# Optimization experiments

Hardware: AMD Instinct MI355X
Metric: run time of the kernel (lower is better)

## Reference

```python
import jax, jax.numpy as jnp
import numpy as np

B, H, W, C = 8, 28, 28, 1024
NH = 16
HD = C // NH          # head dim 64
HID = 4 * C           # mlp hidden 4096
BC = C // 2           # bottleneck channels 512
SCALE = HD ** -0.5


def setup_inputs() -> dict:
    key = jax.random.key(0)
    ks = iter(jax.random.split(key, 32))
    def rn(shape, s=0.02):
        return jax.random.normal(next(ks), shape, jnp.float32) * s
    return dict(
        x=jax.random.normal(next(ks), (B, H, W, C), jnp.float32),
        norm1_w=jnp.ones((C,), jnp.float32), norm1_b=jnp.zeros((C,), jnp.float32),
        qkv_w=rn((C, 3 * C)), qkv_b=jnp.zeros((3 * C,), jnp.float32),
        proj_w=rn((C, C)), proj_b=jnp.zeros((C,), jnp.float32),
        rel_h=rn((2 * H - 1, HD)), rel_w=rn((2 * W - 1, HD)),
        norm2_w=jnp.ones((C,), jnp.float32), norm2_b=jnp.zeros((C,), jnp.float32),
        fc1_w=rn((C, HID)), fc1_b=jnp.zeros((HID,), jnp.float32),
        fc2_w=rn((HID, C)), fc2_b=jnp.zeros((C,), jnp.float32),
        conv1_w=rn((1, 1, C, BC)), ln1_w=jnp.ones((BC,), jnp.float32), ln1_b=jnp.zeros((BC,), jnp.float32),
        conv2_w=rn((3, 3, BC, BC)), ln2_w=jnp.ones((BC,), jnp.float32), ln2_b=jnp.zeros((BC,), jnp.float32),
        conv3_w=rn((1, 1, BC, C)), ln3_w=rn((C,)), ln3_b=rn((C,)),
    )


def _ln(x, w, b, eps):
    # layernorm over last axis (channels in NHWC)
    m = jnp.mean(x, -1, keepdims=True)
    v = jnp.mean((x - m) ** 2, -1, keepdims=True)
    return (x - m) * jax.lax.rsqrt(v + eps) * w + b


def _conv(x, w, pad):
    return jax.lax.conv_general_dilated(
        x, w, (1, 1), pad, dimension_numbers=('NHWC', 'HWIO', 'NHWC'))


def _gelu(x):
    return jax.nn.gelu(x, approximate=False)


def _block_forward(x, norm1_w, norm1_b, qkv_w, qkv_b, proj_w, proj_b,
                   rel_h, rel_w, norm2_w, norm2_b, fc1_w, fc1_b, fc2_w, fc2_b,
                   conv1_w, ln1_w, ln1_b, conv2_w, ln2_w, ln2_b, conv3_w, ln3_w, ln3_b):
    S = H * W
    shortcut = x
    xn = _ln(x, norm1_w, norm1_b, 1e-5)

    # ---- attention with decomposed relative position bias ----
    qkv = xn.reshape(B, S, C) @ qkv_w + qkv_b                 # [B,S,3C]
    qkv = qkv.reshape(B, S, 3, NH, HD).transpose(2, 0, 3, 1, 4)  # [3,B,nh,S,hd]
    q, k, v = qkv[0], qkv[1], qkv[2]
    attn = jnp.einsum('bnsd,bntd->bnst', q * SCALE, k)        # [B,nh,S,S]

    idx_h = jnp.arange(H)[:, None] - jnp.arange(H)[None, :] + (H - 1)
    idx_w = jnp.arange(W)[:, None] - jnp.arange(W)[None, :] + (W - 1)
    Rh = rel_h[idx_h]   # [H,H,hd]
    Rw = rel_w[idx_w]   # [W,W,hd]
    qr = q.reshape(B, NH, H, W, HD)
    bias_h = jnp.einsum('bnhwd,hkd->bnhwk', qr, Rh)           # [B,nh,H,W,H]
    bias_w = jnp.einsum('bnhwd,wkd->bnhwk', qr, Rw)           # [B,nh,H,W,W]
    attn = (attn.reshape(B, NH, H, W, H, W)
            + bias_h[..., :, None] + bias_w[..., None, :]).reshape(B, NH, S, S)

    attn = jax.nn.softmax(attn, axis=-1)
    out = jnp.einsum('bnst,bntd->bnsd', attn, v)              # [B,nh,S,hd]
    out = out.transpose(0, 2, 1, 3).reshape(B, H, W, C)
    out = out @ proj_w + proj_b

    x = shortcut + out

    # ---- MLP ----
    xn = _ln(x, norm2_w, norm2_b, 1e-5)
    x = x + (_gelu(xn.reshape(B, S, C) @ fc1_w + fc1_b) @ fc2_w + fc2_b).reshape(B, H, W, C)

    # ---- residual bottleneck conv (channel LayerNorm, eps=1e-6) ----
    out = _conv(x, conv1_w, 'VALID')
    out = _gelu(_ln(out, ln1_w, ln1_b, 1e-6))
    out = _conv(out, conv2_w, ((1, 1), (1, 1)))
    out = _gelu(_ln(out, ln2_w, ln2_b, 1e-6))
    out = _conv(out, conv3_w, 'VALID')
    out = _ln(out, ln3_w, ln3_b, 1e-6)
    return x + out


def reference(x, norm1_w, norm1_b, qkv_w, qkv_b, proj_w, proj_b,
              rel_h, rel_w, norm2_w, norm2_b, fc1_w, fc1_b, fc2_w, fc2_b,
              conv1_w, ln1_w, ln1_b, conv2_w, ln2_w, ln2_b, conv3_w, ln3_w, ln3_b):
    return _block_forward(x, norm1_w, norm1_b, qkv_w, qkv_b, proj_w, proj_b,
                          rel_h, rel_w, norm2_w, norm2_b, fc1_w, fc1_b, fc2_w, fc2_b,
                          conv1_w, ln1_w, ln1_b, conv2_w, ln2_w, ln2_b, conv3_w, ln3_w, ln3_b)
```

## Files before the change

### kernel.cpp

```cpp
#include <hip/hip_runtime.h>
#include <cstdint>
#include <cstddef>

using u16 = unsigned short;
using u32 = unsigned int;

__device__ __forceinline__ float bf2f(u16 u){
  union { u32 i; float f; } x; x.i = ((u32)u) << 16; return x.f;
}
__device__ __forceinline__ u16 f2bf(float f){
  union { float f; u32 i; } x; x.f = f;
  u32 r = x.i + 0x7fffu + ((x.i >> 16) & 1u);
  return (u16)(r >> 16);
}
__device__ __forceinline__ float gelu_f(float x){
  return 0.5f * x * (1.0f + erff(x * 0.70710678118654752f));
}
__device__ __forceinline__ void gld16(const void* g, void* l){
  __builtin_amdgcn_global_load_lds((__attribute__((address_space(1))) void*)(void*)g,
                                   (__attribute__((address_space(3))) void*)l, 16, 0, 0);
}

typedef __bf16 bf16x8 __attribute__((ext_vector_type(8)));
typedef float  f32x4  __attribute__((ext_vector_type(4)));
typedef u16    u16x4  __attribute__((ext_vector_type(4)));

__global__ __launch_bounds__(256) void k_transpose(const float* __restrict__ src,
                                                   u16* __restrict__ dst, int R, int C){
  __shared__ u16 tile[32][33];
  int bx = blockIdx.x * 32;
  int by = blockIdx.y * 32;
  int tx = threadIdx.x & 31;
  int ty = threadIdx.x >> 5;
  for (int r = ty; r < 32; r += 8)
    tile[r][tx] = f2bf(src[(size_t)(by + r) * C + bx + tx]);
  __syncthreads();
  for (int r = ty; r < 32; r += 8)
    dst[(size_t)(bx + r) * R + by + tx] = tile[tx][r];
}

template<bool IN_F32, bool DO_GELU>
__global__ __launch_bounds__(256) void k_layernorm(const void* __restrict__ inp,
    const float* __restrict__ w, const float* __restrict__ bsh,
    u16* __restrict__ out, int cols, float eps){
  int row = blockIdx.x, t = threadIdx.x;
  size_t base = (size_t)row * cols;
  const float* inf = (const float*)inp;
  const u16*  inb = (const u16*)inp;
  float v[4];
  int ep = cols >> 8;
  float s = 0.f, ss = 0.f;
  for (int e = 0; e < ep; ++e){
    int idx = t + (e << 8);
    float x = IN_F32 ? inf[base + idx] : bf2f(inb[base + idx]);
    v[e] = x; s += x; ss += x * x;
  }
#pragma unroll
  for (int off = 1; off < 64; off <<= 1){
    s  += __shfl_xor(s, off, 64);
    ss += __shfl_xor(ss, off, 64);
  }
  __shared__ float red[8];
  int wv = t >> 6;
  if ((t & 63) == 0){ red[wv] = s; red[4 + wv] = ss; }
  __syncthreads();
  s  = red[0] + red[1] + red[2] + red[3];
  ss = red[4] + red[5] + red[6] + red[7];
  float inv = 1.f / (float)cols;
  float mean = s * inv;
  float var = ss * inv - mean * mean;
  float rs = rsqrtf(var + eps);
  for (int e = 0; e < ep; ++e){
    int idx = t + (e << 8);
    float y = (v[e] - mean) * rs * w[idx] + bsh[idx];
    if (DO_GELU) y = gelu_f(y);
    out[base + idx] = f2bf(y);
  }
}

__global__ __launch_bounds__(256) void k_final(const u16* __restrict__ c3,
    const u16* __restrict__ x2, const float* __restrict__ w,
    const float* __restrict__ bsh, float* __restrict__ out){
  int row = blockIdx.x, t = threadIdx.x;
  size_t base = (size_t)row << 10;
  float v[4];
  float s = 0.f, ss = 0.f;
#pragma unroll
  for (int e = 0; e < 4; ++e){
    int idx = t + (e << 8);
    float x = bf2f(c3[base + idx]);
    v[e] = x; s += x; ss += x * x;
  }
#pragma unroll
  for (int off = 1; off < 64; off <<= 1){
    s  += __shfl_xor(s, off, 64);
    ss += __shfl_xor(ss, off, 64);
  }
  __shared__ float red[8];
  int wv = t >> 6;
  if ((t & 63) == 0){ red[wv] = s; red[4 + wv] = ss; }
  __syncthreads();
  s  = red[0] + red[1] + red[2] + red[3];
  ss = red[4] + red[5] + red[6] + red[7];
  float mean = s * (1.f/1024.f);
  float var = ss * (1.f/1024.f) - mean * mean;
  float rs = rsqrtf(var + 1e-6f);
#pragma unroll
  for (int e = 0; e < 4; ++e){
    int idx = t + (e << 8);
    float y = (v[e] - mean) * rs * w[idx] + bsh[idx];
    out[base + idx] = bf2f(x2[base + idx]) + y;
  }
}

template<int DEPTH, bool BIAS, bool GELU, bool RES, bool OUTB, bool OUTF, bool CONV>
__global__ __launch_bounds__(256, 2) void k_gemm(
    const u16* __restrict__ A, const u16* __restrict__ Bt,
    const float* __restrict__ bias, const float* __restrict__ resf,
    u16* __restrict__ outb, float* __restrict__ outf,
    const u16* __restrict__ zb, int N, int K)
{
  __shared__ __align__(16) u16 smem[DEPTH * 2 * 128 * 32];
  u16* Asb = smem;
  u16* Bsb = smem + DEPTH * 4096;
  int t = threadIdx.x, lane = t & 63, wv = t >> 6;

  int nbx = gridDim.x;
  int nwg = nbx * gridDim.y;
  int li  = blockIdx.y * nbx + blockIdx.x;
  int qc = nwg >> 3, rc = nwg & 7;
  int xcd = li & 7, jj = li >> 3;
  int wg = (xcd < rc ? xcd * (qc + 1) : rc * (qc + 1) + (xcd - rc) * qc) + jj;
  int byy = wg / nbx;
  int bxx = wg - byy * nbx;
  int m0 = byy << 7, n0 = bxx << 7;

  int wm = (wv >> 1) << 6, wn = (wv & 1) << 6;

  f32x4 acc[4][4];
  const f32x4 z4 = {0.f, 0.f, 0.f, 0.f};
#pragma unroll
  for (int i = 0; i < 4; ++i)
#pragma unroll
    for (int j = 0; j < 4; ++j) acc[i][j] = z4;

  int srow = (wv << 5) + (lane >> 2);
  int skp  = (lane & 3) << 3;
  const u16* Ag = A  + (size_t)(m0 + srow) * K + skp;
  const u16* Bg = Bt + (size_t)(n0 + srow) * K + skp;
  const size_t rowskip = (size_t)16 * K;

  int bb0 = 0, h0 = 0, w0 = 0, bb1 = 0, h1 = 0, w1 = 0;
  if (CONV){
    int p0 = m0 + srow;
    bb0 = p0 / 784; int s0i = p0 - bb0 * 784; h0 = s0i / 28; w0 = s0i - h0 * 28;
    int p1 = p0 + 16;
    bb1 = p1 / 784; int s1i = p1 - bb1 * 784; h1 = s1i / 28; w1 = s1i - h1 * 28;
  }

  int fr = lane & 15, fq = (lane >> 4) << 3;

  auto stage = [&](int buf, int k0){
    u16* a0 = Asb + buf * 4096 + (wv << 5) * 32;
    u16* b0 = Bsb + buf * 4096 + (wv << 5) * 32;
    if (CONV){
      int tap = k0 >> 9;
      int ky = tap / 3, kx = tap - ky * 3;
      int ci = (k0 & 511) + skp;
      int hh0 = h0 + ky - 1, ww0 = w0 + kx - 1;
      int hh1 = h1 + ky - 1, ww1 = w1 + kx - 1;
      const u16* s0 = ((unsigned)hh0 < 28u && (unsigned)ww0 < 28u)
          ? A + (((size_t)(bb0 * 28 + hh0)) * 28 + ww0) * 512 + ci : zb;
      const u16* s1 = ((unsigned)hh1 < 28u && (unsigned)ww1 < 28u)
          ? A + (((size_t)(bb1 * 28 + hh1)) * 28 + ww1) * 512 + ci : zb;
      gld16(s0, a0);
      gld16(s1, a0 + 16 * 32);
    } else {
      gld16(Ag + k0, a0);
      gld16(Ag + rowskip + k0, a0 + 16 * 32);
    }
    gld16(Bg + k0, b0);
    gld16(Bg + rowskip + k0, b0 + 16 * 32);
  };

  auto compute = [&](int buf){
    const u16* As = Asb + buf * 4096;
    const u16* Bs = Bsb + buf * 4096;
    bf16x8 af[4], bfr[4];
#pragma unroll
    for (int i = 0; i < 4; ++i)
      af[i] = *(const bf16x8*)&As[(wm + i * 16 + fr) * 32 + fq];
#pragma unroll
    for (int j = 0; j < 4; ++j)
      bfr[j] = *(const bf16x8*)&Bs[(wn + j * 16 + fr) * 32 + fq];
#pragma unroll
    for (int i = 0; i < 4; ++i)
#pragma unroll
      for (int j = 0; j < 4; ++j)
        acc[i][j] = __builtin_amdgcn_mfma_f32_16x16x32_bf16(af[i], bfr[j], acc[i][j], 0, 0, 0);
  };

  int nk = K >> 5;
  stage(0, 0);

  for (int kk = 0; kk < nk; ++kk){
    int nxt = kk + 1;
    if (nxt < nk){
      stage(nxt & 1, nxt << 5);
      asm volatile("s_waitcnt vmcnt(4)" ::: "memory");
    } else {
      asm volatile("s_waitcnt vmcnt(0)" ::: "memory");
    }
    __builtin_amdgcn_s_barrier();
    compute(kk & 1);
    __builtin_amdgcn_s_barrier();
  }

  int rr = (lane >> 4) << 2;
  int cc = lane & 15;
  if (OUTB){
    u16* Cs = smem;
#pragma unroll
    for (int i = 0; i < 4; ++i)
#pragma unroll
      for (int j = 0; j < 4; ++j){
        int lc = wn + j * 16 + cc;
        int gc = n0 + lc;
        float bb = BIAS ? bias[gc] : 0.f;
#pragma unroll
        for (int r = 0; r < 4; ++r){
          int lr = wm + i * 16 + rr + r;
          float vv = acc[i][j][r] + bb;
          if (RES) vv += resf[(size_t)(m0 + lr) * N + gc];
          if (GELU) vv = gelu_f(vv);
          Cs[lr * 128 + lc] = f2bf(vv);
        }
      }
    __syncthreads();
#pragma unroll
    for (int it = 0; it < 8; ++it){
      int flat = it * 256 + t;
      int row = flat >> 4;
      int col = (flat & 15) << 3;
      *(uint4*)&outb[(size_t)(m0 + row) * N + n0 + col] = *(const uint4*)&Cs[row * 128 + col];
    }
  } else {
#pragma unroll
    for (int i = 0; i < 4; ++i)
#pragma unroll
      for (int j = 0; j < 4; ++j){
        int gc = n0 + wn + j * 16 + cc;
        float bb = BIAS ? bias[gc] : 0.f;
#pragma unroll
        for (int r = 0; r < 4; ++r){
          int gr = m0 + wm + i * 16 + rr + r;
          size_t idx = (size_t)gr * N + gc;
          float vv = acc[i][j][r] + bb;
          if (RES) vv += resf[idx];
          if (GELU) vv = gelu_f(vv);
          outf[idx] = vv;
        }
      }
  }
}

__global__ __launch_bounds__(256) void k_vtrans(const u16* __restrict__ qkv, u16* __restrict__ vtg){
  __shared__ u32 tile[64][33];
  int bnh = blockIdx.x;
  int st  = blockIdx.y;
  int b = bnh >> 4, nh = bnh & 15;
  int t = threadIdx.x;
  int tx = t & 31;
  int ty = t >> 5;
  const u16* src = qkv + (size_t)b * 784 * 3072 + 2048 + nh * 64;
  int s0 = st << 6;
  for (int r = ty; r < 64; r += 8){
    int s = s0 + r;
    u32 val = 0u;
    if (s < 784) val = *(const u32*)(src + (size_t)s * 3072 + tx * 2);
    tile[r][tx] = val;
  }
  __syncthreads();
  u16* dst = vtg + (size_t)bnh * 64 * 832 + s0;
  for (int d = ty; d < 64; d += 8){
    u32 lo = tile[2 * tx][d >> 1];
    u32 hi = tile[2 * tx + 1][d >> 1];
    u16 a  = (d & 1) ? (u16)(lo >> 16) : (u16)lo;
    u16 bb = (d & 1) ? (u16)(hi >> 16) : (u16)hi;
    u32 pk = (u32)a | ((u32)bb << 16);
    *(u32*)(dst + (size_t)d * 832 + 2 * tx) = pk;
  }
}

#define PST 72
#define GT2 36
#define LOG2E 1.4426950408889634f
__global__ __launch_bounds__(256, 2) void k_attn8(const u16* __restrict__ qkv,
    const float* __restrict__ relh, const float* __restrict__ relw,
    const u16* __restrict__ vtg, u16* __restrict__ out)
{
  __shared__ __align__(16) u16 k_s[2][64 * 64];
  __shared__ __align__(16) u16 v_s[2][64 * 64];
  __shared__ __align__(16) u16 p_s[128 * PST];
  __shared__ __align__(16) u16 gh_t[28 * GT2];
  __shared__ __align__(16) u16 gw_t[28 * GT2];

  const int t = threadIdx.x, lane = t & 63, wv = t >> 6;
  int id = blockIdx.x;
  int xr = id & 7, rest = id >> 3;
  int qt = rest % 7, gg = rest / 7;
  int bnh = xr + (gg << 3);
  const int b = bnh >> 4, nh = bnh & 15;
  const int q0 = qt << 7;
  const size_t rowbase = (size_t)b * 784;
  const int wq0 = wv << 5;
  const int fr = lane & 15;
  const int fq = lane >> 4;

  u16* rh_s = p_s;
  u16* rw_s = p_s + 64 * PST;
  {
    int row = t >> 2, c0 = (t & 3) << 4;
    u16 bh_[16], bw_[16];
    if (row < 55){
      const float* ph = relh + row * 64 + c0;
      const float* pw = relw + row * 64 + c0;
#pragma unroll
      for (int e = 0; e < 16; ++e){ bh_[e] = f2bf(ph[e]); bw_[e] = f2bf(pw[e]); }
    } else {
#pragma unroll
      for (int e = 0; e < 16; ++e){ bh_[e] = 0; bw_[e] = 0; }
    }
    *(uint4*)&rh_s[row * PST + c0]     = *(uint4*)bh_;
    *(uint4*)&rh_s[row * PST + c0 + 8] = *(uint4*)(bh_ + 8);
    *(uint4*)&rw_s[row * PST + c0]     = *(uint4*)bw_;
    *(uint4*)&rw_s[row * PST + c0 + 8] = *(uint4*)(bw_ + 8);
  }

  bf16x8 qf[2][2];
#pragma unroll
  for (int mf = 0; mf < 2; ++mf)
#pragma unroll
    for (int ks = 0; ks < 2; ++ks){
      int row = q0 + wq0 + mf * 16 + fr;
      if (row < 784){
        qf[mf][ks] = *(const bf16x8*)(qkv + (rowbase + row) * 3072 + nh * 64 + fq * 8 + ks * 32);
      } else {
        uint4 z = {0u,0u,0u,0u}; qf[mf][ks] = *(bf16x8*)&z;
      }
    }
  __syncthreads();

  const f32x4 z4 = {0.f,0.f,0.f,0.f};
#pragma unroll
  for (int which = 0; which < 2; ++which){
    const u16* rs = which ? rw_s : rh_s;
    f32x4 G[2][4];
#pragma unroll
    for (int mf = 0; mf < 2; ++mf)
#pragma unroll
      for (int nf = 0; nf < 4; ++nf) G[mf][nf] = z4;
#pragma unroll
    for (int nf = 0; nf < 4; ++nf){
      bf16x8 rf0 = *(const bf16x8*)&rs[(nf * 16 + fr) * PST + fq * 8];
      bf16x8 rf1 = *(const bf16x8*)&rs[(nf * 16 + fr) * PST + fq * 8 + 32];
#pragma unroll
      for (int mf = 0; mf < 2; ++mf){
        G[mf][nf] = __builtin_amdgcn_mfma_f32_16x16x32_bf16(qf[mf][0], rf0, G[mf][nf], 0, 0, 0);
        G[mf][nf] = __builtin_amdgcn_mfma_f32_16x16x32_bf16(qf[mf][1], rf1, G[mf][nf], 0, 0, 0);
      }
    }
    u16* gt = which ? gw_t : gh_t;
#pragma unroll
    for (int mf = 0; mf < 2; ++mf)
#pragma unroll
      for (int r = 0; r < 4; ++r){
        int lr = wq0 + mf * 16 + fq * 4 + r;
        int grow = q0 + lr;
        int hq = grow / 28;
        int coord = which ? (grow - hq * 28) : hq;
#pragma unroll
        for (int nf = 0; nf < 4; ++nf){
          int j = nf * 16 + fr;
          int kk = coord + 27 - j;
          if ((unsigned)kk < 28u) gt[kk * GT2 + lr] = f2bf(G[mf][nf][r] * LOG2E);
        }
      }
  }

  f32x4 acc[2][5];
#pragma unroll
  for (int mf = 0; mf < 2; ++mf)
#pragma unroll
    for (int nf = 0; nf < 5; ++nf) acc[mf][nf] = z4;

  u16 onesu[8];
#pragma unroll
  for (int e = 0; e < 8; ++e) onesu[e] = 0x3f80;
  bf16x8 onesf = *(bf16x8*)onesu;

  const int sr = lane >> 3;
  const int sc = (lane & 7) ^ sr;
  const u16* kstage = qkv + rowbase * 3072 + 1024 + nh * 64;
  const u16* vstage = vtg + (size_t)bnh * 64 * 832;
  const int r0 = (wv << 4) + sr;
  const int swz = (fr & 7);

  auto stageKV = [&](int buf, int kt){
    int ktb = kt << 6;
    int jg0 = ktb + r0;       int jc0 = jg0 < 784 ? jg0 : 783;
    int jg1 = jg0 + 8;        int jc1 = jg1 < 784 ? jg1 : 783;
    u16* kd = &k_s[buf][(wv << 4) * 64];
    u16* vd = &v_s[buf][(wv << 4) * 64];
    gld16(kstage + (size_t)jc0 * 3072 + (sc << 3), kd);
    gld16(kstage + (size_t)jc1 * 3072 + (sc << 3), kd + 8 * 64);
    gld16(vstage + (size_t)r0 * 832 + ktb + (sc << 3), vd);
    gld16(vstage + (size_t)(r0 + 8) * 832 + ktb + (sc << 3), vd + 8 * 64);
  };

  stageKV(0, 0);
  asm volatile("s_waitcnt lgkmcnt(0)" ::: "memory");
  __builtin_amdgcn_s_barrier();

  const float SSC = 0.125f * LOG2E;

  for (int kt = 0; kt < 13; ++kt){
    if (kt < 12){
      stageKV((kt + 1) & 1, kt + 1);
      asm volatile("s_waitcnt vmcnt(4)" ::: "memory");
    } else {
      asm volatile("s_waitcnt vmcnt(0)" ::: "memory");
    }
    __builtin_amdgcn_s_barrier();

    const u16* ks = k_s[kt & 1];
    const u16* vs = v_s[kt & 1];
    const int ktb = kt << 6;

    f32x4 S[2][4];
#pragma unroll
    for (int nf = 0; nf < 4; ++nf){
      int rb = (nf * 16 + fr) << 6;
      bf16x8 kf0 = *(const bf16x8*)&ks[rb + ((fq ^ swz) << 3)];
      bf16x8 kf1 = *(const bf16x8*)&ks[rb + (((fq + 4) ^ swz) << 3)];
#pragma unroll
      for (int mf = 0; mf < 2; ++mf){
        f32x4 s = z4;
        s = __builtin_amdgcn_mfma_f32_16x16x32_bf16(qf[mf][0], kf0, s, 0, 0, 0);
        s = __builtin_amdgcn_mfma_f32_16x16x32_bf16(qf[mf][1], kf1, s, 0, 0, 0);
        S[mf][nf] = s;
      }
    }

    int hj[4], wj[4]; bool val[4];
#pragma unroll
    for (int nf = 0; nf < 4; ++nf){
      int jg = ktb + nf * 16 + fr;
      int h = jg / 28;
      hj[nf] = h; wj[nf] = jg - h * 28; val[nf] = (jg < 784);
    }

#pragma unroll
    for (int mf = 0; mf < 2; ++mf){
      int lrb = wq0 + mf * 16 + fq * 4;
#pragma unroll
      for (int nf = 0; nf < 4; ++nf){
        u16x4 h4 = *(const u16x4*)&gh_t[hj[nf] * GT2 + lrb];
        u16x4 w4 = *(const u16x4*)&gw_t[wj[nf] * GT2 + lrb];
#pragma unroll
        for (int r = 0; r < 4; ++r){
          float p = 0.f;
          if (val[nf])
            p = exp2f(fmaf(SSC, S[mf][nf][r], bf2f(h4[r]) + bf2f(w4[r])));
          p_s[(lrb + r) * PST + nf * 16 + fr] = f2bf(p);
        }
      }
    }

#pragma unroll
    for (int ks2 = 0; ks2 < 2; ++ks2){
      bf16x8 pf0 = *(const bf16x8*)&p_s[(wq0 + fr) * PST + fq * 8 + ks2 * 32];
      bf16x8 pf1 = *(const bf16x8*)&p_s[(wq0 + 16 + fr) * PST + fq * 8 + ks2 * 32];
#pragma unroll
      for (int nf = 0; nf < 4; ++nf){
        bf16x8 vf = *(const bf16x8*)&vs[((nf * 16 + fr) << 6) + (((fq + ks2 * 4) ^ swz) << 3)];
        acc[0][nf] = __builtin_amdgcn_mfma_f32_16x16x32_bf16(pf0, vf, acc[0][nf], 0, 0, 0);
        acc[1][nf] = __builtin_amdgcn_mfma_f32_16x16x32_bf16(pf1, vf, acc[1][nf], 0, 0, 0);
      }
      acc[0][4] = __builtin_amdgcn_mfma_f32_16x16x32_bf16(pf0, onesf, acc[0][4], 0, 0, 0);
      acc[1][4] = __builtin_amdgcn_mfma_f32_16x16x32_bf16(pf1, onesf, acc[1][4], 0, 0, 0);
    }
    __builtin_amdgcn_s_barrier();
  }

  u16* Os = &k_s[0][0];
#pragma unroll
  for (int mf = 0; mf < 2; ++mf)
#pragma unroll
    for (int r = 0; r < 4; ++r){
      int lr = wq0 + mf * 16 + fq * 4 + r;
      float inv = 1.f / acc[mf][4][r];
#pragma unroll
      for (int nf = 0; nf < 4; ++nf)
        Os[lr * 64 + nf * 16 + fr] = f2bf(acc[mf][nf][r] * inv);
    }
  __syncthreads();
#pragma unroll
  for (int it = 0; it < 4; ++it){
    int flat = it * 256 + t;
    int row = flat >> 3;
    int col = (flat & 7) << 3;
    int grow = q0 + row;
    if (grow < 784)
      *(uint4*)&out[(rowbase + grow) * 1024 + nh * 64 + col] = *(const uint4*)&Os[row * 64 + col];
  }
}

extern "C" void kernel_launch(void* const* d_in, const int* in_sizes, int n_in,
                              void* d_out, int out_size, void* d_ws, size_t ws_size,
                              hipStream_t stream)
{
  (void)in_sizes; (void)n_in; (void)out_size; (void)ws_size;
  const float* x      = (const float*)d_in[0];
  const float* n1w    = (const float*)d_in[1];
  const float* n1b    = (const float*)d_in[2];
  const float* qkv_w  = (const float*)d_in[3];
  const float* qkv_b  = (const float*)d_in[4];
  const float* proj_w = (const float*)d_in[5];
  const float* proj_b = (const float*)d_in[6];
  const float* rel_h  = (const float*)d_in[7];
  const float* rel_w  = (const float*)d_in[8];
  const float* n2w    = (const float*)d_in[9];
  const float* n2b    = (const float*)d_in[10];
  const float* fc1_w  = (const float*)d_in[11];
  const float* fc1_b  = (const float*)d_in[12];
  const float* fc2_w  = (const float*)d_in[13];
  const float* fc2_b  = (const float*)d_in[14];
  const float* c1w    = (const float*)d_in[15];
  const float* l1w    = (const float*)d_in[16];
  const float* l1b    = (const float*)d_in[17];
  const float* c2w    = (const float*)d_in[18];
  const float* l2w    = (const float*)d_in[19];
  const float* l2b    = (const float*)d_in[20];
  const float* c3w    = (const float*)d_in[21];
  const float* l3w    = (const float*)d_in[22];
  const float* l3b    = (const float*)d_in[23];

  char* ws = (char*)d_ws;
  size_t off = 0;
  auto alloc = [&](size_t bytes) -> void* {
    void* p = ws + off; off += (bytes + 255) & ~(size_t)255; return p;
  };
  const size_t M = 6272;
  u16* qkvT  = (u16*)alloc((size_t)3072 * 1024 * 2);
  u16* projT = (u16*)alloc((size_t)1024 * 1024 * 2);
  u16* fc1T  = (u16*)alloc((size_t)4096 * 1024 * 2);
  u16* fc2T  = (u16*)alloc((size_t)1024 * 4096 * 2);
  u16* c1T   = (u16*)alloc((size_t)512 * 1024 * 2);
  u16* c2T   = (u16*)alloc((size_t)512 * 4608 * 2);
  u16* c3T   = (u16*)alloc((size_t)1024 * 512 * 2);
  u16* qkvbuf = (u16*)alloc(M * 3072 * 2);
  u16* attn   = (u16*)alloc(M * 1024 * 2);
  u16* xn     = (u16*)alloc(M * 1024 * 2);
  float* x1   = (float*)alloc(M * 1024 * 4);
  u16* x2b    = (u16*)alloc(M * 1024 * 2);
  u16* c1buf  = (u16*)alloc(M * 512 * 2);
  u16* g1buf  = (u16*)alloc(M * 512 * 2);
  u16* zbuf   = (u16*)alloc(256);
  u16* hmlp   = qkvbuf;
  u16* xn2    = xn;
  u16* c2buf  = c1buf;
  u16* g2buf  = g1buf;
  u16* c3buf  = attn;
  u16* vtg    = (u16*)x1;

  hipMemsetAsync(zbuf, 0, 256, stream);

  dim3 blk(256);
  k_transpose<<<dim3(3072/32, 1024/32), blk, 0, stream>>>(qkv_w, qkvT, 1024, 3072);
  k_transpose<<<dim3(1024/32, 1024/32), blk, 0, stream>>>(proj_w, projT, 1024, 1024);
  k_transpose<<<dim3(4096/32, 1024/32), blk, 0, stream>>>(fc1_w, fc1T, 1024, 4096);
  k_transpose<<<dim3(1024/32, 4096/32), blk, 0, stream>>>(fc2_w, fc2T, 4096, 1024);
  k_transpose<<<dim3(512/32, 1024/32),  blk, 0, stream>>>(c1w, c1T, 1024, 512);
  k_transpose<<<dim3(512/32, 4608/32),  blk, 0, stream>>>(c2w, c2T, 4608, 512);
  k_transpose<<<dim3(1024/32, 512/32),  blk, 0, stream>>>(c3w, c3T, 512, 1024);

  k_layernorm<true,false><<<6272, blk, 0, stream>>>(x, n1w, n1b, xn, 1024, 1e-5f);
  k_gemm<2,true,false,false,true,false,false><<<dim3(24,49), blk, 0, stream>>>(
      xn, qkvT, qkv_b, nullptr, qkvbuf, nullptr, nullptr, 3072, 1024);
  k_vtrans<<<dim3(128, 13), blk, 0, stream>>>(qkvbuf, vtg);
  k_attn8<<<896, blk, 0, stream>>>(qkvbuf, rel_h, rel_w, vtg, attn);
  k_gemm<2,true,false,true,false,true,false><<<dim3(8,49), blk, 0, stream>>>(
      attn, projT, proj_b, x, nullptr, x1, nullptr, 1024, 1024);
  k_layernorm<true,false><<<6272, blk, 0, stream>>>(x1, n2w, n2b, xn2, 1024, 1e-5f);
  k_gemm<2,true,true,false,true,false,false><<<dim3(32,49), blk, 0, stream>>>(
      xn2, fc1T, fc1_b, nullptr, hmlp, nullptr, nullptr, 4096, 1024);
  k_gemm<2,true,false,true,true,false,false><<<dim3(8,49), blk, 0, stream>>>(
      hmlp, fc2T, fc2_b, x1, x2b, nullptr, nullptr, 1024, 4096);
  k_gemm<2,false,false,false,true,false,false><<<dim3(4,49), blk, 0, stream>>>(
      x2b, c1T, nullptr, nullptr, c1buf, nullptr, nullptr, 512, 1024);
  k_layernorm<false,true><<<6272, blk, 0, stream>>>(c1buf, l1w, l1b, g1buf, 512, 1e-6f);
  k_gemm<2,false,false,false,true,false,true><<<dim3(4,49), blk, 0, stream>>>(
      g1buf, c2T, nullptr, nullptr, c2buf, nullptr, zbuf, 512, 4608);
  k_layernorm<false,true><<<6272, blk, 0, stream>>>(c2buf, l2w, l2b, g2buf, 512, 1e-6f);
  k_gemm<2,false,false,false,true,false,false><<<dim3(8,49), blk, 0, stream>>>(
      g2buf, c3T, nullptr, nullptr, c3buf, nullptr, nullptr, 1024, 512);
  k_final<<<6272, blk, 0, stream>>>(c3buf, x2b, l3w, l3b, (float*)d_out);
}
```

Measured before the change: 665.7 us.

## Merge weight transposes into one launch and group GEMM tile order by row bands

Replaces the seven separate weight-transpose launches with one kernel that takes a table of segments and picks its matrix from the block index, removing per-launch overhead and tail gaps. Separately, the GEMM tile mapping now walks blocks column-major within groups of eight M-rows instead of plain row-major, so that concurrently running workgroups share A and B tiles in L2. The segment lookup adds a small per-block branch cost, and the remapping changes cache behaviour for every GEMM.

```diff
diff --git a/kernel.cpp b/kernel.cpp
--- a/kernel.cpp
+++ b/kernel.cpp
@@ -25,18 +25,31 @@
 typedef float  f32x4  __attribute__((ext_vector_type(4)));
 typedef u16    u16x4  __attribute__((ext_vector_type(4)));
 
-__global__ __launch_bounds__(256) void k_transpose(const float* __restrict__ src,
-                                                   u16* __restrict__ dst, int R, int C){
+struct TSeg { const float* src; u16* dst; int R; int C; int tx; int start; };
+struct TSegs { TSeg s[7]; };
+
+__global__ __launch_bounds__(256) void k_transpose_all(TSegs segs){
   __shared__ u16 tile[32][33];
-  int bx = blockIdx.x * 32;
-  int by = blockIdx.y * 32;
-  int tx = threadIdx.x & 31;
-  int ty = threadIdx.x >> 5;
+  int bid = blockIdx.x;
+  const float* src = segs.s[0].src; u16* dst = segs.s[0].dst;
+  int R = segs.s[0].R, C = segs.s[0].C, tx = segs.s[0].tx, loc = bid;
+#pragma unroll
+  for (int i = 1; i < 7; ++i){
+    if (bid >= segs.s[i].start){
+      src = segs.s[i].src; dst = segs.s[i].dst;
+      R = segs.s[i].R; C = segs.s[i].C; tx = segs.s[i].tx;
+      loc = bid - segs.s[i].start;
+    }
+  }
+  int byt = loc / tx, bxt = loc - byt * tx;
+  int bx = bxt << 5, by = byt << 5;
+  int txi = threadIdx.x & 31;
+  int ty  = threadIdx.x >> 5;
   for (int r = ty; r < 32; r += 8)
-    tile[r][tx] = f2bf(src[(size_t)(by + r) * C + bx + tx]);
+    tile[r][txi] = f2bf(src[(size_t)(by + r) * C + bx + txi]);
   __syncthreads();
   for (int r = ty; r < 32; r += 8)
-    dst[(size_t)(bx + r) * R + by + tx] = tile[tx][r];
+    dst[(size_t)(bx + r) * R + by + txi] = tile[txi][r];
 }
 
 template<bool IN_F32, bool DO_GELU>
@@ -126,13 +139,18 @@
   int t = threadIdx.x, lane = t & 63, wv = t >> 6;
 
   int nbx = gridDim.x;
-  int nwg = nbx * gridDim.y;
+  int nby = gridDim.y;
+  int nwg = nbx * nby;
   int li  = blockIdx.y * nbx + blockIdx.x;
   int qc = nwg >> 3, rc = nwg & 7;
   int xcd = li & 7, jj = li >> 3;
   int wg = (xcd < rc ? xcd * (qc + 1) : rc * (qc + 1) + (xcd - rc) * qc) + jj;
-  int byy = wg / nbx;
-  int bxx = wg - byy * nbx;
+  int wpg = nbx << 3;
+  int g   = wg / wpg;
+  int r8  = wg - g * wpg;
+  int rows = nby - (g << 3); rows = rows < 8 ? rows : 8;
+  int bxx = r8 / rows;
+  int byy = (g << 3) + (r8 - bxx * rows);
   int m0 = byy << 7, n0 = bxx << 7;
 
   int wm = (wv >> 1) << 6, wn = (wv & 1) << 6;
@@ -577,13 +595,20 @@
   hipMemsetAsync(zbuf, 0, 256, stream);
 
   dim3 blk(256);
-  k_transpose<<<dim3(3072/32, 1024/32), blk, 0, stream>>>(qkv_w, qkvT, 1024, 3072);
-  k_transpose<<<dim3(1024/32, 1024/32), blk, 0, stream>>>(proj_w, projT, 1024, 1024);
-  k_transpose<<<dim3(4096/32, 1024/32), blk, 0, stream>>>(fc1_w, fc1T, 1024, 4096);
-  k_transpose<<<dim3(1024/32, 4096/32), blk, 0, stream>>>(fc2_w, fc2T, 4096, 1024);
-  k_transpose<<<dim3(512/32, 1024/32),  blk, 0, stream>>>(c1w, c1T, 1024, 512);
-  k_transpose<<<dim3(512/32, 4608/32),  blk, 0, stream>>>(c2w, c2T, 4608, 512);
-  k_transpose<<<dim3(1024/32, 512/32),  blk, 0, stream>>>(c3w, c3T, 512, 1024);
+  TSegs segs;
+  int tstart = 0;
+  auto addseg = [&](int i, const float* s, u16* d, int R, int C){
+    segs.s[i] = TSeg{ s, d, R, C, C >> 5, tstart };
+    tstart += (C >> 5) * (R >> 5);
+  };
+  addseg(0, qkv_w, qkvT, 1024, 3072);
+  addseg(1, proj_w, projT, 1024, 1024);
+  addseg(2, fc1_w, fc1T, 1024, 4096);
+  addseg(3, fc2_w, fc2T, 4096, 1024);
+  addseg(4, c1w, c1T, 1024, 512);
+  addseg(5, c2w, c2T, 4608, 512);
+  addseg(6, c3w, c3T, 512, 1024);
+  k_transpose_all<<<tstart, blk, 0, stream>>>(segs);
 
   k_layernorm<true,false><<<6272, blk, 0, stream>>>(x, n1w, n1b, xn, 1024, 1e-5f);
   k_gemm<2,true,false,false,true,false,false><<<dim3(24,49), blk, 0, stream>>>(
```

Result: no change. 656.2 us (-1.4%).
